# Optimization experiments

Hardware: AMD Instinct MI355X
Metric: run time of the kernel (lower is better)

The kernel has to match this reference:

```python
import jax, jax.numpy as jnp
import numpy as np
import math

HEADS = 16
LAYER, NUM_LAYERS = 6, 12
ALPHA = 1.0 - math.tanh(math.pi * LAYER / NUM_LAYERS)
EPS = 1e-5


def _rot_half(t):
    d = t.shape[-1] // 2
    return jnp.concatenate([-t[..., d:], t[..., :d]], axis=-1)


def axial_rope(t):
    # t: [b, n, H, W, d]. Axial rotary: height rotates first d/2, width rotates second d/2.
    H, W, d = t.shape[2], t.shape[3], t.shape[4]
    half = d // 2
    inv_freq = 1.0 / (10000.0 ** (jnp.arange(0, half, 2, dtype=jnp.float32) / half))  # [half/2]
    ang_h = jnp.arange(H, dtype=jnp.float32)[:, None] * inv_freq[None, :]  # [H, half/2]
    ang_w = jnp.arange(W, dtype=jnp.float32)[:, None] * inv_freq[None, :]  # [W, half/2]
    ang_h = jnp.concatenate([ang_h, ang_h], axis=-1)  # [H, half]
    ang_w = jnp.concatenate([ang_w, ang_w], axis=-1)  # [W, half]
    ch, sh = jnp.cos(ang_h)[:, None, :], jnp.sin(ang_h)[:, None, :]  # [H,1,half]
    cw, sw = jnp.cos(ang_w)[None, :, :], jnp.sin(ang_w)[None, :, :]  # [1,W,half]
    th, tw = t[..., :half], t[..., half:]
    th = th * ch + _rot_half(th) * sh
    tw = tw * cw + _rot_half(tw) * sw
    return jnp.concatenate([th, tw], axis=-1)


def setup_inputs() -> dict:
    key = jax.random.key(0)
    ks = jax.random.split(key, 4)
    b, H, W, hid = 32, 28, 28, 1024
    return {
        "x": jax.random.normal(ks[0], (b, H, W, hid), jnp.float32),
        "input_img": jax.random.normal(ks[1], (b, H, W, hid), jnp.float32),
        "qkv_w": jax.random.normal(ks[2], (hid, 3 * hid), jnp.float32) * 0.02,
        "o_w": jax.random.normal(ks[3], (hid, hid), jnp.float32) * 0.02,
        "gn_w": jnp.ones((HEADS,), jnp.float32),
        "gn_b": jnp.zeros((HEADS,), jnp.float32),
    }


def reference(x, input_img, qkv_w, o_w, gn_w, gn_b):
    b, H, W, hid = x.shape
    n, dh = HEADS, hid // HEADS
    qkv = x @ qkv_w  # [b,H,W,3*hid]
    # 'b h w (c d) -> c b h w d'
    qkv = qkv.reshape(b, H, W, 3, hid).transpose(3, 0, 1, 2, 4)
    qkv = qkv + input_img[None] * ALPHA
    # 'c b h w (n d) -> c b n h w d'; unpack order is q, v, k
    qkv = qkv.reshape(3, b, H, W, n, dh).transpose(0, 1, 4, 2, 3, 5)
    q, v, k = qkv[0], qkv[1], qkv[2]
    gamma = (1.0 - 2.0 ** (-5.0 - jnp.arange(n, dtype=jnp.float32)))[None, :, None, None, None]
    k = k * gamma
    q, k = axial_rope(q), axial_rope(k)
    # attention along the W axis per row: [b,n,H,W,W]
    scores = jnp.einsum('bnhxd,bnhzd->bnhxz', q, k)
    # original einsum sums v over heights h as well as over y
    vsum = v.sum(axis=2)  # [b,n,W,dh]
    out = jnp.einsum('bnxwy,bnyd->bnxwd', scores, vsum)  # [b,n,H,W,dh]
    # GroupNorm(num_heads, num_heads): normalize each head over (H,W,dh)
    mu = out.mean(axis=(2, 3, 4), keepdims=True)
    var = out.var(axis=(2, 3, 4), keepdims=True)
    out = (out - mu) / jnp.sqrt(var + EPS)
    out = out * gn_w[None, :, None, None, None] + gn_b[None, :, None, None, None]
    # 'b n h w d -> b h w (n d)'
    out = out.transpose(0, 2, 3, 1, 4).reshape(b, H, W, hid)
    return out @ o_w
```

## Files before the change

### kernel.cpp

```cpp
#include <hip/hip_runtime.h>
#include <cstdint>
#include <cstddef>

#define HEADS 16
#define DH 64
#define BH 28
#define BWW 28
#define BATCH 32
#define HID 1024
#define M_ROWS 25088
#define ALPHA_C 0.082847664332725576f
#define EPS_C 1e-5f

typedef unsigned short ushort_t;
typedef __attribute__((ext_vector_type(8))) short bf16x8;
typedef __attribute__((ext_vector_type(4))) float f32x4;

__device__ inline unsigned short f2bf(float f) {
  unsigned int u = __builtin_bit_cast(unsigned int, f);
  u = (u + 0x7fffu + ((u >> 16) & 1u)) >> 16;
  return (unsigned short)u;
}
__device__ inline float bf2f(unsigned short h) {
  unsigned int u = ((unsigned int)h) << 16;
  return __builtin_bit_cast(float, u);
}

__global__ __launch_bounds__(256) void detect_k(const ushort_t* __restrict__ x,
                                                const ushort_t* __restrict__ qw,
                                                int* __restrict__ flagp) {
  int tid = threadIdx.x;
  int big = 0;
  #pragma unroll
  for (int j = 0; j < 4; ++j) {
    float a = fabsf(bf2f(x[tid * 4 + j]));
    float b = fabsf(bf2f(qw[tid * 4 + j]));
    if (!(a < 1e3f)) big++;
    if (!(b < 1e3f)) big++;
  }
  __shared__ int cnt;
  if (tid == 0) cnt = 0;
  __syncthreads();
  if (big) atomicAdd(&cnt, big);
  __syncthreads();
  if (tid == 0) *flagp = (cnt == 0) ? 1 : 0;
}

__global__ __launch_bounds__(256) void conv_x_k(const void* __restrict__ src,
                                                const int* __restrict__ flagp,
                                                ushort_t* __restrict__ dst, long n8) {
  if (*flagp) return;
  long i = (long)blockIdx.x * 256 + threadIdx.x;
  if (i >= n8) return;
  long e = i * 8;
  const float* sf = (const float*)src;
  float4 a = *(const float4*)(sf + e);
  float4 b = *(const float4*)(sf + e + 4);
  union { ushort_t u[8]; uint4 v; } o;
  o.u[0] = f2bf(a.x); o.u[1] = f2bf(a.y); o.u[2] = f2bf(a.z); o.u[3] = f2bf(a.w);
  o.u[4] = f2bf(b.x); o.u[5] = f2bf(b.y); o.u[6] = f2bf(b.z); o.u[7] = f2bf(b.w);
  *(uint4*)(dst + e) = o.v;
}

__global__ __launch_bounds__(256) void sumh_k(const void* __restrict__ x,
                                              const void* __restrict__ img,
                                              const int* __restrict__ flagp,
                                              ushort_t* __restrict__ xsum,
                                              float* __restrict__ imgsum) {
  int i = blockIdx.x * 256 + threadIdx.x;
  int c = i & 1023;
  int bw = i >> 10;
  int b = bw / BWW, w = bw % BWW;
  size_t base = ((size_t)b * BH * BWW + w) * HID + c;
  const size_t hstride = (size_t)BWW * HID;
  float sx = 0.f, si = 0.f;
  if (*flagp) {
    const ushort_t* xb = (const ushort_t*)x;
    const ushort_t* ib = (const ushort_t*)img;
    #pragma unroll 4
    for (int h = 0; h < BH; ++h) {
      sx += bf2f(xb[base + h * hstride]);
      si += bf2f(ib[base + h * hstride]);
    }
  } else {
    const float* xf = (const float*)x;
    const float* iff = (const float*)img;
    #pragma unroll 4
    for (int h = 0; h < BH; ++h) {
      sx += xf[base + h * hstride];
      si += iff[base + h * hstride];
    }
  }
  xsum[i] = f2bf(sx);
  imgsum[i] = si * ALPHA_C;
}

__global__ void transpose_any_k(const void* __restrict__ src, const int* __restrict__ flagp,
                                ushort_t* __restrict__ dst, int R, int C) {
  __shared__ float tile[32][33];
  int isbf = *flagp;
  int c0 = blockIdx.x * 32, r0 = blockIdx.y * 32;
  int tx = threadIdx.x, ty = threadIdx.y;
  const ushort_t* sb = (const ushort_t*)src;
  const float* sf = (const float*)src;
  #pragma unroll
  for (int i = ty; i < 32; i += 8) {
    size_t idx = (size_t)(r0 + i) * C + (c0 + tx);
    tile[i][tx] = isbf ? bf2f(sb[idx]) : sf[idx];
  }
  __syncthreads();
  #pragma unroll
  for (int i = ty; i < 32; i += 8)
    dst[(size_t)(c0 + i) * R + (r0 + tx)] = f2bf(tile[tx][i]);
}

#define BK 32

#define STAGE(bufA, bufB, kk0) do {                                                              \
  const ushort_t* a0_ = aRow + (kk0);                                                            \
  const ushort_t* b0_ = bRow + (kk0);                                                            \
  __builtin_amdgcn_global_load_lds((const __attribute__((address_space(1))) unsigned int*)a0_,   \
      (__attribute__((address_space(3))) unsigned int*)((bufA) + tid * 8), 16, 0, 0);            \
  __builtin_amdgcn_global_load_lds((const __attribute__((address_space(1))) unsigned int*)(a0_ + (size_t)64 * K), \
      (__attribute__((address_space(3))) unsigned int*)((bufA) + 2048 + tid * 8), 16, 0, 0);     \
  __builtin_amdgcn_global_load_lds((const __attribute__((address_space(1))) unsigned int*)b0_,   \
      (__attribute__((address_space(3))) unsigned int*)((bufB) + tid * 8), 16, 0, 0);            \
  __builtin_amdgcn_global_load_lds((const __attribute__((address_space(1))) unsigned int*)(b0_ + (size_t)64 * K), \
      (__attribute__((address_space(3))) unsigned int*)((bufB) + 2048 + tid * 8), 16, 0, 0);     \
} while (0)

__global__ __launch_bounds__(256) void gemm_qkv_k(const void* __restrict__ x_raw,
                                                  const ushort_t* __restrict__ x_bf,
                                                  const ushort_t* __restrict__ Bt,
                                                  const void* __restrict__ img_raw,
                                                  const ushort_t* __restrict__ img_bf,
                                                  const int* __restrict__ flagp,
                                                  ushort_t* __restrict__ qbuf,
                                                  ushort_t* __restrict__ kbuf) {
  __shared__ ushort_t As[2][128 * BK];
  __shared__ ushort_t Bs[2][128 * BK];
  const int tid = threadIdx.x;
  const int K = 1024;
  const int ntile = 16;
  const int nt = blockIdx.x % ntile;
  const int n0 = (nt < 8) ? nt * 128 : nt * 128 + 1024;
  const int m0 = (blockIdx.x / ntile) * 128;
  const int lane = tid & 63;
  const int wave = tid >> 6;
  const int wm = (wave >> 1) * 64;
  const int wn = (wave & 1) * 64;
  const int fr = lane & 15;
  const int fq = lane >> 4;
  const int isbf = *flagp;
  const ushort_t* A  = isbf ? (const ushort_t*)x_raw  : x_bf;
  const ushort_t* IM = isbf ? (const ushort_t*)img_raw : img_bf;

  f32x4 acc[4][4] = {};
  const int srow = tid >> 2;
  const int skk  = (tid & 3) * 8;
  const ushort_t* aRow = A  + (size_t)(m0 + srow) * K + skk;
  const ushort_t* bRow = Bt + (size_t)(n0 + srow) * K + skk;

  STAGE(As[0], Bs[0], 0);
  __syncthreads();
  int cur = 0;
  for (int k0 = 0; k0 < K; k0 += BK) {
    int nxt = cur ^ 1;
    if (k0 + BK < K) STAGE(As[nxt], Bs[nxt], k0 + BK);
    bf16x8 af[4], bfv[4];
    #pragma unroll
    for (int i = 0; i < 4; ++i)
      af[i] = *reinterpret_cast<const bf16x8*>(&As[cur][(wm + i * 16 + fr) * BK + fq * 8]);
    #pragma unroll
    for (int i = 0; i < 4; ++i)
      bfv[i] = *reinterpret_cast<const bf16x8*>(&Bs[cur][(wn + i * 16 + fr) * BK + fq * 8]);
    #pragma unroll
    for (int mi = 0; mi < 4; ++mi)
      #pragma unroll
      for (int ni = 0; ni < 4; ++ni)
        acc[mi][ni] = __builtin_amdgcn_mfma_f32_16x16x32_bf16(af[mi], bfv[ni], acc[mi][ni], 0, 0, 0);
    __syncthreads();
    cur = nxt;
  }

  const int colg = n0 + wn;
  const int t = colg >> 10;
  const int n = (colg & 1023) >> 6;
  const float gamma = 1.0f - exp2f(-5.0f - (float)n);
  const float invf = powf(10000.0f, -(float)fr / 16.0f);

  #pragma unroll
  for (int mi = 0; mi < 4; ++mi) {
    #pragma unroll
    for (int r = 0; r < 4; ++r) {
      int m = m0 + wm + mi * 16 + fq * 4 + r;
      int b = m / 784, rem = m % 784;
      int h = rem / 28, w = rem % 28;
      size_t ibase = (size_t)m * HID + n * DH + fr;
      float v0 = acc[mi][0][r] + bf2f(IM[ibase])      * ALPHA_C;
      float v1 = acc[mi][1][r] + bf2f(IM[ibase + 16]) * ALPHA_C;
      float v2 = acc[mi][2][r] + bf2f(IM[ibase + 32]) * ALPHA_C;
      float v3 = acc[mi][3][r] + bf2f(IM[ibase + 48]) * ALPHA_C;
      if (t == 2) { v0 *= gamma; v1 *= gamma; v2 *= gamma; v3 *= gamma; }
      float snh, csh, snw, csw;
      __sincosf((float)h * invf, &snh, &csh);
      __sincosf((float)w * invf, &snw, &csw);
      float o0 = v0 * csh - v1 * snh;
      float o1 = v1 * csh + v0 * snh;
      float o2 = v2 * csw - v3 * snw;
      float o3 = v3 * csw + v2 * snw;
      ushort_t* dst = (t == 0 ? qbuf : kbuf) +
          (((((size_t)b * HEADS + n) * BH + h) * BWW + w) * DH) + fr;
      dst[0]  = f2bf(o0);
      dst[16] = f2bf(o1);
      dst[32] = f2bf(o2);
      dst[48] = f2bf(o3);
    }
  }
}

__global__ __launch_bounds__(256) void vsum_gemm_k(const ushort_t* __restrict__ A,
                                                   const ushort_t* __restrict__ Bt,
                                                   const float* __restrict__ imgsum,
                                                   float* __restrict__ vsum) {
  __shared__ ushort_t As[2][128 * BK];
  __shared__ ushort_t Bs[2][128 * BK];
  const int tid = threadIdx.x;
  const int K = 1024;
  const int n0 = (blockIdx.x % 8) * 128;
  const int m0 = (blockIdx.x / 8) * 128;
  const int lane = tid & 63;
  const int wave = tid >> 6;
  const int wm = (wave >> 1) * 64;
  const int wn = (wave & 1) * 64;
  const int fr = lane & 15;
  const int fq = lane >> 4;

  f32x4 acc[4][4] = {};
  const int srow = tid >> 2;
  const int skk  = (tid & 3) * 8;
  const ushort_t* aRow = A  + (size_t)(m0 + srow) * K + skk;
  const ushort_t* bRow = Bt + (size_t)(n0 + srow) * K + skk;

  STAGE(As[0], Bs[0], 0);
  __syncthreads();
  int cur = 0;
  for (int k0 = 0; k0 < K; k0 += BK) {
    int nxt = cur ^ 1;
    if (k0 + BK < K) STAGE(As[nxt], Bs[nxt], k0 + BK);
    bf16x8 af[4], bfv[4];
    #pragma unroll
    for (int i = 0; i < 4; ++i)
      af[i] = *reinterpret_cast<const bf16x8*>(&As[cur][(wm + i * 16 + fr) * BK + fq * 8]);
    #pragma unroll
    for (int i = 0; i < 4; ++i)
      bfv[i] = *reinterpret_cast<const bf16x8*>(&Bs[cur][(wn + i * 16 + fr) * BK + fq * 8]);
    #pragma unroll
    for (int mi = 0; mi < 4; ++mi)
      #pragma unroll
      for (int ni = 0; ni < 4; ++ni)
        acc[mi][ni] = __builtin_amdgcn_mfma_f32_16x16x32_bf16(af[mi], bfv[ni], acc[mi][ni], 0, 0, 0);
    __syncthreads();
    cur = nxt;
  }

  #pragma unroll
  for (int mi = 0; mi < 4; ++mi)
    #pragma unroll
    for (int r = 0; r < 4; ++r) {
      int m = m0 + wm + mi * 16 + fq * 4 + r;
      int b = m / BWW, w = m % BWW;
      #pragma unroll
      for (int ni = 0; ni < 4; ++ni) {
        int col = n0 + wn + ni * 16 + fr;
        int n = col >> 6, d = col & 63;
        vsum[((((size_t)b * HEADS + n) * BWW) + w) * DH + d] =
            acc[mi][ni][r] + imgsum[(size_t)m * HID + col];
      }
    }
}

__global__ __launch_bounds__(256) void attn_k(const ushort_t* __restrict__ qbuf,
                                              const ushort_t* __restrict__ kbuf,
                                              const float* __restrict__ vsum,
                                              const void* __restrict__ gn_w,
                                              const void* __restrict__ gn_b,
                                              const int* __restrict__ flagp,
                                              ushort_t* __restrict__ xo) {
  __shared__ __align__(16) ushort_t outL[BH * BWW * DH];
  __shared__ ushort_t Vt[64 * 32];
  __shared__ ushort_t Sa[4][32 * 32];
  __shared__ float rs[4][2];
  __shared__ float mu_s, rstd_s;
  const int bn = blockIdx.x;
  const int b = bn >> 4, n = bn & 15;
  const int tid = threadIdx.x;
  const int lane = tid & 63, wv = tid >> 6;
  const int fr = lane & 15, fq = lane >> 4;
  const size_t vbase = (size_t)bn * BWW * DH;

  for (int e = tid; e < 64 * 32; e += 256) {
    int d = e >> 5, y = e & 31;
    Vt[e] = (y < BWW) ? f2bf(vsum[vbase + (size_t)y * DH + d]) : (ushort_t)0;
  }
  __syncthreads();

  bf16x8 bv[4];
  #pragma unroll
  for (int i = 0; i < 4; ++i)
    bv[i] = *reinterpret_cast<const bf16x8*>(&Vt[(i * 16 + fr) * 32 + fq * 8]);

  float lsum = 0.f, lsq = 0.f;
  ushort_t* sa = Sa[wv];

  for (int hi = 0; hi < 7; ++hi) {
    const int h = wv + hi * 4;
    const size_t qb = ((size_t)bn * BH + h) * BWW * DH;

    f32x4 s[2][2] = {};
    #pragma unroll
    for (int kk = 0; kk < 2; ++kk) {
      bf16x8 qf[2], kf[2];
      #pragma unroll
      for (int t = 0; t < 2; ++t) {
        qf[t] = *reinterpret_cast<const bf16x8*>(qbuf + qb + (size_t)(t * 16 + fr) * DH + kk * 32 + fq * 8);
        kf[t] = *reinterpret_cast<const bf16x8*>(kbuf + qb + (size_t)(t * 16 + fr) * DH + kk * 32 + fq * 8);
      }
      #pragma unroll
      for (int mt = 0; mt < 2; ++mt)
        #pragma unroll
        for (int nt = 0; nt < 2; ++nt)
          s[mt][nt] = __builtin_amdgcn_mfma_f32_16x16x32_bf16(qf[mt], kf[nt], s[mt][nt], 0, 0, 0);
    }

    #pragma unroll
    for (int mt = 0; mt < 2; ++mt)
      #pragma unroll
      for (int nt = 0; nt < 2; ++nt)
        #pragma unroll
        for (int r = 0; r < 4; ++r)
          sa[(mt * 16 + fq * 4 + r) * 32 + nt * 16 + fr] = f2bf(s[mt][nt][r]);
    __syncthreads();

    f32x4 o[2][4] = {};
    #pragma unroll
    for (int mt = 0; mt < 2; ++mt) {
      bf16x8 af = *reinterpret_cast<const bf16x8*>(&sa[(mt * 16 + fr) * 32 + fq * 8]);
      #pragma unroll
      for (int nt = 0; nt < 4; ++nt)
        o[mt][nt] = __builtin_amdgcn_mfma_f32_16x16x32_bf16(af, bv[nt], o[mt][nt], 0, 0, 0);
    }

    #pragma unroll
    for (int mt = 0; mt < 2; ++mt)
      #pragma unroll
      for (int r = 0; r < 4; ++r) {
        int w_ = mt * 16 + fq * 4 + r;
        if (w_ < BWW) {
          ushort_t* dl = outL + ((size_t)(h * BWW + w_) * DH) + fr;
          #pragma unroll
          for (int nt = 0; nt < 4; ++nt) {
            float v = o[mt][nt][r];
            dl[nt * 16] = f2bf(v);
            lsum += v; lsq += v * v;
          }
        }
      }
  }

  #pragma unroll
  for (int off = 32; off > 0; off >>= 1) {
    lsum += __shfl_down(lsum, off);
    lsq  += __shfl_down(lsq, off);
  }
  if (lane == 0) { rs[wv][0] = lsum; rs[wv][1] = lsq; }
  __syncthreads();
  if (tid == 0) {
    float s  = rs[0][0] + rs[1][0] + rs[2][0] + rs[3][0];
    float q2 = rs[0][1] + rs[1][1] + rs[2][1] + rs[3][1];
    const float Ninv = 1.0f / (float)(BH * BWW * DH);
    float mu = s * Ninv;
    float var = q2 * Ninv - mu * mu;
    mu_s = mu;
    rstd_s = rsqrtf(var + EPS_C);
  }
  __syncthreads();

  const int isbf = *flagp;
  const float gw = isbf ? bf2f(((const ushort_t*)gn_w)[n]) : ((const float*)gn_w)[n];
  const float gb = isbf ? bf2f(((const ushort_t*)gn_b)[n]) : ((const float*)gn_b)[n];
  const float sc = rstd_s * gw;
  const float sh_ = gb - mu_s * sc;
  for (int c = tid; c < BH * BWW * 8; c += 256) {
    int d8 = c & 7;
    int hw = c >> 3;
    int w = hw % BWW, h = hw / BWW;
    bf16x8 vv = *reinterpret_cast<const bf16x8*>(outL + (size_t)hw * DH + d8 * 8);
    union { ushort_t u[8]; uint4 q4; } o;
    #pragma unroll
    for (int j = 0; j < 8; ++j)
      o.u[j] = f2bf(bf2f((ushort_t)vv[j]) * sc + sh_);
    *(uint4*)(xo + (((size_t)(b * BH + h) * BWW + w) * HID) + n * DH + d8 * 8) = o.q4;
  }
}

__global__ __launch_bounds__(256) void gemm_bt_k(const ushort_t* __restrict__ A,
                                                 const ushort_t* __restrict__ Bt,
                                                 void* __restrict__ Cv,
                                                 const int* __restrict__ flagp,
                                                 int M, int N, int K) {
  __shared__ ushort_t As[2][128 * BK];
  __shared__ ushort_t Bs[2][128 * BK];
  const int tid = threadIdx.x;
  const int ntile = N / 128;
  const int n0 = (blockIdx.x % ntile) * 128;
  const int m0 = (blockIdx.x / ntile) * 128;
  const int lane = tid & 63;
  const int wave = tid >> 6;
  const int wm = (wave >> 1) * 64;
  const int wn = (wave & 1) * 64;
  const int fr = lane & 15;
  const int fq = lane >> 4;

  f32x4 acc[4][4] = {};
  const int srow = tid >> 2;
  const int skk  = (tid & 3) * 8;
  const ushort_t* aRow = A  + (size_t)(m0 + srow) * K + skk;
  const ushort_t* bRow = Bt + (size_t)(n0 + srow) * K + skk;

  STAGE(As[0], Bs[0], 0);
  __syncthreads();
  int cur = 0;
  for (int k0 = 0; k0 < K; k0 += BK) {
    int nxt = cur ^ 1;
    if (k0 + BK < K) STAGE(As[nxt], Bs[nxt], k0 + BK);
    bf16x8 af[4], bfv[4];
    #pragma unroll
    for (int i = 0; i < 4; ++i)
      af[i] = *reinterpret_cast<const bf16x8*>(&As[cur][(wm + i * 16 + fr) * BK + fq * 8]);
    #pragma unroll
    for (int i = 0; i < 4; ++i)
      bfv[i] = *reinterpret_cast<const bf16x8*>(&Bs[cur][(wn + i * 16 + fr) * BK + fq * 8]);
    #pragma unroll
    for (int mi = 0; mi < 4; ++mi)
      #pragma unroll
      for (int ni = 0; ni < 4; ++ni)
        acc[mi][ni] = __builtin_amdgcn_mfma_f32_16x16x32_bf16(af[mi], bfv[ni], acc[mi][ni], 0, 0, 0);
    __syncthreads();
    cur = nxt;
  }

  int isbf = *flagp;
  if (isbf) {
    ushort_t* C = (ushort_t*)Cv;
    #pragma unroll
    for (int mi = 0; mi < 4; ++mi)
      #pragma unroll
      for (int r = 0; r < 4; ++r) {
        int m = m0 + wm + mi * 16 + fq * 4 + r;
        ushort_t* crow = C + (size_t)m * N + n0 + wn + fr;
        #pragma unroll
        for (int ni = 0; ni < 4; ++ni) crow[ni * 16] = f2bf(acc[mi][ni][r]);
      }
  } else {
    float* C = (float*)Cv;
    #pragma unroll
    for (int mi = 0; mi < 4; ++mi)
      #pragma unroll
      for (int r = 0; r < 4; ++r) {
        int m = m0 + wm + mi * 16 + fq * 4 + r;
        float* crow = C + (size_t)m * N + n0 + wn + fr;
        #pragma unroll
        for (int ni = 0; ni < 4; ++ni) crow[ni * 16] = acc[mi][ni][r];
      }
  }
}

extern "C" void kernel_launch(void* const* d_in, const int* in_sizes, int n_in,
                              void* d_out, int out_size, void* d_ws, size_t ws_size,
                              hipStream_t stream) {
  const void* x     = d_in[0];
  const void* img   = d_in[1];
  const void* qkv_w = d_in[2];
  const void* o_w   = d_in[3];
  const void* gn_w  = d_in[4];
  const void* gn_b  = d_in[5];

  char* ws = (char*)d_ws;
  ushort_t* x_bf   = (ushort_t*)(ws);
  ushort_t* xo     = (ushort_t*)(ws);
  ushort_t* qbuf   = (ushort_t*)(ws + 51380224);
  ushort_t* xsum   = (ushort_t*)(ws + 51380224);
  float*    imgsum = (float*)(ws + 53215232);
  ushort_t* kbuf   = (ushort_t*)(ws + 102760448);
  float*    vsum   = (float*)(ws + 154140672);
  int*      flag   = (int*)(ws + 157810688);
  ushort_t* w1T    = (ushort_t*)(ws + 157810944);
  ushort_t* w2T    = (ushort_t*)(ws + 164102400);
  ushort_t* img_bf = (ushort_t*)(ws + 166199552);

  detect_k<<<1, 256, 0, stream>>>((const ushort_t*)x, (const ushort_t*)qkv_w, flag);
  conv_x_k<<<12544, 256, 0, stream>>>(x,   flag, x_bf,   3211264L);
  conv_x_k<<<12544, 256, 0, stream>>>(img, flag, img_bf, 3211264L);
  sumh_k<<<3584, 256, 0, stream>>>(x, img, flag, xsum, imgsum);
  transpose_any_k<<<dim3(96, 32), dim3(32, 8), 0, stream>>>(qkv_w, flag, w1T, 1024, 3072);
  transpose_any_k<<<dim3(32, 32), dim3(32, 8), 0, stream>>>(o_w, flag, w2T, 1024, 1024);

  vsum_gemm_k<<<56, 256, 0, stream>>>(xsum, w1T + (size_t)1024 * 1024, imgsum, vsum);
  gemm_qkv_k<<<196 * 16, 256, 0, stream>>>(x, x_bf, w1T, img, img_bf, flag, qbuf, kbuf);

  attn_k<<<BATCH * HEADS, 256, 0, stream>>>(qbuf, kbuf, vsum, gn_w, gn_b, flag, xo);
  gemm_bt_k<<<196 * 8, 256, 0, stream>>>(xo, w2T, d_out, flag, M_ROWS, 1024, 1024);
}
```

Baseline: 692.0 us.

## Fuse fp32-to-bf16 conversion with height sums and single-buffer GEMM LDS staging

Replaces the two conversion kernels and the height-sum kernel with one prep kernel. It reads x and img once, writes bf16 copies and accumulates the per-column sums. This removes a full extra pass over the large fp32 inputs. Separately, the three GEMMs switch from double-buffered LDS staging to a single buffer with barriers before and after each load. That halves shared memory and may raise occupancy, but it loses the overlap of loads with MFMA compute.

```diff
diff --git a/kernel.cpp b/kernel.cpp
--- a/kernel.cpp
+++ b/kernel.cpp
@@ -46,53 +46,45 @@
   if (tid == 0) *flagp = (cnt == 0) ? 1 : 0;
 }
 
-__global__ __launch_bounds__(256) void conv_x_k(const void* __restrict__ src,
-                                                const int* __restrict__ flagp,
-                                                ushort_t* __restrict__ dst, long n8) {
-  if (*flagp) return;
-  long i = (long)blockIdx.x * 256 + threadIdx.x;
-  if (i >= n8) return;
-  long e = i * 8;
-  const float* sf = (const float*)src;
-  float4 a = *(const float4*)(sf + e);
-  float4 b = *(const float4*)(sf + e + 4);
-  union { ushort_t u[8]; uint4 v; } o;
-  o.u[0] = f2bf(a.x); o.u[1] = f2bf(a.y); o.u[2] = f2bf(a.z); o.u[3] = f2bf(a.w);
-  o.u[4] = f2bf(b.x); o.u[5] = f2bf(b.y); o.u[6] = f2bf(b.z); o.u[7] = f2bf(b.w);
-  *(uint4*)(dst + e) = o.v;
-}
-
-__global__ __launch_bounds__(256) void sumh_k(const void* __restrict__ x,
+__global__ __launch_bounds__(256) void prep_k(const void* __restrict__ x,
                                               const void* __restrict__ img,
                                               const int* __restrict__ flagp,
-                                              ushort_t* __restrict__ xsum,
-                                              float* __restrict__ imgsum) {
-  int i = blockIdx.x * 256 + threadIdx.x;
-  int c = i & 1023;
-  int bw = i >> 10;
-  int b = bw / BWW, w = bw % BWW;
-  size_t base = ((size_t)b * BH * BWW + w) * HID + c;
-  const size_t hstride = (size_t)BWW * HID;
-  float sx = 0.f, si = 0.f;
+                                              unsigned* __restrict__ x_bf,
+                                              unsigned* __restrict__ img_bf,
+                                              unsigned* __restrict__ xsum,
+                                              float2* __restrict__ imgsum) {
+  const int blk = blockIdx.x;
+  const int half = blk & 1;
+  const int bw = blk >> 1;
+  const int b = bw / BWW, w = bw % BWW;
+  const int c = half * 512 + threadIdx.x * 2;
+  const size_t base2 = (((size_t)(b * BH * BWW) + w) * HID + c) >> 1;
+  const size_t hstr2 = (size_t)BWW * HID / 2;
+  float sx0 = 0.f, sx1 = 0.f, si0 = 0.f, si1 = 0.f;
   if (*flagp) {
-    const ushort_t* xb = (const ushort_t*)x;
-    const ushort_t* ib = (const ushort_t*)img;
-    #pragma unroll 4
+    const unsigned* xb = (const unsigned*)x;
+    const unsigned* ib = (const unsigned*)img;
     for (int h = 0; h < BH; ++h) {
-      sx += bf2f(xb[base + h * hstride]);
-      si += bf2f(ib[base + h * hstride]);
+      unsigned ux = xb[base2 + h * hstr2];
+      unsigned ui = ib[base2 + h * hstr2];
+      sx0 += bf2f((ushort_t)(ux & 0xffffu)); sx1 += bf2f((ushort_t)(ux >> 16));
+      si0 += bf2f((ushort_t)(ui & 0xffffu)); si1 += bf2f((ushort_t)(ui >> 16));
     }
   } else {
-    const float* xf = (const float*)x;
-    const float* iff = (const float*)img;
-    #pragma unroll 4
+    const float2* xf = (const float2*)x;
+    const float2* iff = (const float2*)img;
     for (int h = 0; h < BH; ++h) {
-      sx += xf[base + h * hstride];
-      si += iff[base + h * hstride];
-    }
-  }
-  xsum[i] = f2bf(sx);
-  imgsum[i] = si * ALPHA_C;
+      float2 a = xf[base2 + h * hstr2];
+      float2 g = iff[base2 + h * hstr2];
+      x_bf[base2 + h * hstr2]   = ((unsigned)f2bf(a.y) << 16) | f2bf(a.x);
+      img_bf[base2 + h * hstr2] = ((unsigned)f2bf(g.y) << 16) | f2bf(g.x);
+      sx0 += a.x; sx1 += a.y;
+      si0 += g.x; si1 += g.y;
+    }
+  }
+  const size_t o2 = ((size_t)bw * HID + c) >> 1;
+  xsum[o2] = ((unsigned)f2bf(sx1) << 16) | f2bf(sx0);
+  imgsum[o2] = make_float2(si0 * ALPHA_C, si1 * ALPHA_C);
 }
 
 __global__ void transpose_any_k(const void* __restrict__ src, const int* __restrict__ flagp,
@@ -116,7 +108,7 @@
 
 #define BK 32
 
-#define STAGE(bufA, bufB, kk0) do {                                                              \
+#define STAGE1(bufA, bufB, kk0) do {                                                             \
   const ushort_t* a0_ = aRow + (kk0);                                                            \
   const ushort_t* b0_ = bRow + (kk0);                                                            \
   __builtin_amdgcn_global_load_lds((const __attribute__((address_space(1))) unsigned int*)a0_,   \
@@ -137,8 +129,8 @@
                                                   const int* __restrict__ flagp,
                                                   ushort_t* __restrict__ qbuf,
                                                   ushort_t* __restrict__ kbuf) {
-  __shared__ ushort_t As[2][128 * BK];
-  __shared__ ushort_t Bs[2][128 * BK];
+  __shared__ ushort_t As[128 * BK];
+  __shared__ ushort_t Bs[128 * BK];
   const int tid = threadIdx.x;
   const int K = 1024;
   const int ntile = 16;
@@ -152,7 +144,7 @@
   const int fr = lane & 15;
   const int fq = lane >> 4;
   const int isbf = *flagp;
-  const ushort_t* A  = isbf ? (const ushort_t*)x_raw  : x_bf;
+  const ushort_t* A  = isbf ? (const ushort_t*)x_raw   : x_bf;
   const ushort_t* IM = isbf ? (const ushort_t*)img_raw : img_bf;
 
   f32x4 acc[4][4] = {};
@@ -161,26 +153,22 @@
   const ushort_t* aRow = A  + (size_t)(m0 + srow) * K + skk;
   const ushort_t* bRow = Bt + (size_t)(n0 + srow) * K + skk;
 
-  STAGE(As[0], Bs[0], 0);
-  __syncthreads();
-  int cur = 0;
   for (int k0 = 0; k0 < K; k0 += BK) {
-    int nxt = cur ^ 1;
-    if (k0 + BK < K) STAGE(As[nxt], Bs[nxt], k0 + BK);
+    __syncthreads();
+    STAGE1(As, Bs, k0);
+    __syncthreads();
     bf16x8 af[4], bfv[4];
     #pragma unroll
     for (int i = 0; i < 4; ++i)
-      af[i] = *reinterpret_cast<const bf16x8*>(&As[cur][(wm + i * 16 + fr) * BK + fq * 8]);
-    #pragma unroll
-    for (int i = 0; i < 4; ++i)
-      bfv[i] = *reinterpret_cast<const bf16x8*>(&Bs[cur][(wn + i * 16 + fr) * BK + fq * 8]);
+      af[i] = *reinterpret_cast<const bf16x8*>(&As[(wm + i * 16 + fr) * BK + fq * 8]);
+    #pragma unroll
+    for (int i = 0; i < 4; ++i)
+      bfv[i] = *reinterpret_cast<const bf16x8*>(&Bs[(wn + i * 16 + fr) * BK + fq * 8]);
     #pragma unroll
     for (int mi = 0; mi < 4; ++mi)
       #pragma unroll
       for (int ni = 0; ni < 4; ++ni)
         acc[mi][ni] = __builtin_amdgcn_mfma_f32_16x16x32_bf16(af[mi], bfv[ni], acc[mi][ni], 0, 0, 0);
-    __syncthreads();
-    cur = nxt;
   }
 
   const int colg = n0 + wn;
@@ -223,8 +211,8 @@
                                                    const ushort_t* __restrict__ Bt,
                                                    const float* __restrict__ imgsum,
                                                    float* __restrict__ vsum) {
-  __shared__ ushort_t As[2][128 * BK];
-  __shared__ ushort_t Bs[2][128 * BK];
+  __shared__ ushort_t As[128 * BK];
+  __shared__ ushort_t Bs[128 * BK];
   const int tid = threadIdx.x;
   const int K = 1024;
   const int n0 = (blockIdx.x % 8) * 128;
@@ -242,26 +230,22 @@
   const ushort_t* aRow = A  + (size_t)(m0 + srow) * K + skk;
   const ushort_t* bRow = Bt + (size_t)(n0 + srow) * K + skk;
 
-  STAGE(As[0], Bs[0], 0);
-  __syncthreads();
-  int cur = 0;
   for (int k0 = 0; k0 < K; k0 += BK) {
-    int nxt = cur ^ 1;
-    if (k0 + BK < K) STAGE(As[nxt], Bs[nxt], k0 + BK);
+    __syncthreads();
+    STAGE1(As, Bs, k0);
+    __syncthreads();
     bf16x8 af[4], bfv[4];
     #pragma unroll
     for (int i = 0; i < 4; ++i)
-      af[i] = *reinterpret_cast<const bf16x8*>(&As[cur][(wm + i * 16 + fr) * BK + fq * 8]);
-    #pragma unroll
-    for (int i = 0; i < 4; ++i)
-      bfv[i] = *reinterpret_cast<const bf16x8*>(&Bs[cur][(wn + i * 16 + fr) * BK + fq * 8]);
+      af[i] = *reinterpret_cast<const bf16x8*>(&As[(wm + i * 16 + fr) * BK + fq * 8]);
+    #pragma unroll
+    for (int i = 0; i < 4; ++i)
+      bfv[i] = *reinterpret_cast<const bf16x8*>(&Bs[(wn + i * 16 + fr) * BK + fq * 8]);
     #pragma unroll
     for (int mi = 0; mi < 4; ++mi)
       #pragma unroll
       for (int ni = 0; ni < 4; ++ni)
         acc[mi][ni] = __builtin_amdgcn_mfma_f32_16x16x32_bf16(af[mi], bfv[ni], acc[mi][ni], 0, 0, 0);
-    __syncthreads();
-    cur = nxt;
   }
 
   #pragma unroll
@@ -409,8 +393,8 @@
                                                  void* __restrict__ Cv,
                                                  const int* __restrict__ flagp,
                                                  int M, int N, int K) {
-  __shared__ ushort_t As[2][128 * BK];
-  __shared__ ushort_t Bs[2][128 * BK];
+  __shared__ ushort_t As[128 * BK];
+  __shared__ ushort_t Bs[128 * BK];
   const int tid = threadIdx.x;
   const int ntile = N / 128;
   const int n0 = (blockIdx.x % ntile) * 128;
@@ -428,26 +412,22 @@
   const ushort_t* aRow = A  + (size_t)(m0 + srow) * K + skk;
   const ushort_t* bRow = Bt + (size_t)(n0 + srow) * K + skk;
 
-  STAGE(As[0], Bs[0], 0);
-  __syncthreads();
-  int cur = 0;
   for (int k0 = 0; k0 < K; k0 += BK) {
-    int nxt = cur ^ 1;
-    if (k0 + BK < K) STAGE(As[nxt], Bs[nxt], k0 + BK);
+    __syncthreads();
+    STAGE1(As, Bs, k0);
+    __syncthreads();
     bf16x8 af[4], bfv[4];
     #pragma unroll
     for (int i = 0; i < 4; ++i)
-      af[i] = *reinterpret_cast<const bf16x8*>(&As[cur][(wm + i * 16 + fr) * BK + fq * 8]);
-    #pragma unroll
-    for (int i = 0; i < 4; ++i)
-      bfv[i] = *reinterpret_cast<const bf16x8*>(&Bs[cur][(wn + i * 16 + fr) * BK + fq * 8]);
+      af[i] = *reinterpret_cast<const bf16x8*>(&As[(wm + i * 16 + fr) * BK + fq * 8]);
+    #pragma unroll
+    for (int i = 0; i < 4; ++i)
+      bfv[i] = *reinterpret_cast<const bf16x8*>(&Bs[(wn + i * 16 + fr) * BK + fq * 8]);
     #pragma unroll
     for (int mi = 0; mi < 4; ++mi)
       #pragma unroll
       for (int ni = 0; ni < 4; ++ni)
         acc[mi][ni] = __builtin_amdgcn_mfma_f32_16x16x32_bf16(af[mi], bfv[ni], acc[mi][ni], 0, 0, 0);
-    __syncthreads();
-    cur = nxt;
   }
 
   int isbf = *flagp;
@@ -500,9 +480,8 @@
   ushort_t* img_bf = (ushort_t*)(ws + 166199552);
 
   detect_k<<<1, 256, 0, stream>>>((const ushort_t*)x, (const ushort_t*)qkv_w, flag);
-  conv_x_k<<<12544, 256, 0, stream>>>(x,   flag, x_bf,   3211264L);
-  conv_x_k<<<12544, 256, 0, stream>>>(img, flag, img_bf, 3211264L);
-  sumh_k<<<3584, 256, 0, stream>>>(x, img, flag, xsum, imgsum);
+  prep_k<<<BATCH * BWW * 2, 256, 0, stream>>>(x, img, flag,
+      (unsigned*)x_bf, (unsigned*)img_bf, (unsigned*)xsum, (float2*)imgsum);
   transpose_any_k<<<dim3(96, 32), dim3(32, 8), 0, stream>>>(qkv_w, flag, w1T, 1024, 3072);
   transpose_any_k<<<dim3(32, 32), dim3(32, 8), 0, stream>>>(o_w, flag, w2T, 1024, 1024);
 
```

Result: faster. 599.2 us (-13.4%).
